# Kernel tuning notes

Measured on AMD Instinct MI355X. Metric: run time of the kernel, lower is better.

The kernel has to match this reference:

```python
import jax, jax.numpy as jnp
import numpy as np

N_NODES = 100000
N_EDGES = 1600000
IN_FEATS = 64
HIDDEN = 64
TOPO_DIM = 16
NUM_CLASSES = 4
NUM_GRAPHS = 64


def setup_inputs() -> dict:
    key = jax.random.key(0)
    ks = jax.random.split(key, 10)
    x = jax.random.normal(ks[0], (N_NODES, IN_FEATS), dtype=jnp.float32)
    edge_index = jax.random.randint(ks[1], (2, N_EDGES), 0, N_NODES, dtype=jnp.int64)
    batch = jnp.sort(jax.random.randint(ks[2], (N_NODES,), 0, NUM_GRAPHS, dtype=jnp.int64))
    topo = jax.random.normal(ks[3], (NUM_GRAPHS, TOPO_DIM), dtype=jnp.float32)
    # GCNConv weights (glorot-ish scale) and biases
    W1 = jax.random.normal(ks[4], (IN_FEATS, HIDDEN), dtype=jnp.float32) / np.sqrt(IN_FEATS)
    b1 = jnp.zeros((HIDDEN,), dtype=jnp.float32)
    W2 = jax.random.normal(ks[5], (HIDDEN, HIDDEN), dtype=jnp.float32) / np.sqrt(HIDDEN)
    b2 = jnp.zeros((HIDDEN,), dtype=jnp.float32)
    Wlin = jax.random.normal(ks[6], (HIDDEN + TOPO_DIM, NUM_CLASSES), dtype=jnp.float32) / np.sqrt(HIDDEN + TOPO_DIM)
    blin = jnp.zeros((NUM_CLASSES,), dtype=jnp.float32)
    return {"x": x, "edge_index": edge_index, "batch": batch, "topo": topo,
            "W1": W1, "b1": b1, "W2": W2, "b2": b2, "Wlin": Wlin, "blin": blin}


def _gcn_conv(x, W, b, src, dst, deg_inv_sqrt):
    # PyG GCNConv: add self-loops, symmetric normalization D^-1/2 (A+I) D^-1/2, then linear.
    xw = x @ W                                   # [N, H]
    norm = deg_inv_sqrt[src] * deg_inv_sqrt[dst]  # [E]
    msgs = xw[src] * norm[:, None]               # gather + scale, [E, H]
    agg = jax.ops.segment_sum(msgs, dst, num_segments=x.shape[0])
    # self-loop contribution: norm_ii = deg_inv_sqrt[i]^2
    agg = agg + xw * (deg_inv_sqrt * deg_inv_sqrt)[:, None]
    return agg + b


def reference(x, edge_index, batch, topo, W1, b1, W2, b2, Wlin, blin):
    src, dst = edge_index[0], edge_index[1]
    n = x.shape[0]
    # degree including self-loop
    deg = jax.ops.segment_sum(jnp.ones_like(dst, dtype=x.dtype), dst, num_segments=n) + 1.0
    deg_inv_sqrt = jax.lax.rsqrt(deg)
    h = jax.nn.relu(_gcn_conv(x, W1, b1, src, dst, deg_inv_sqrt))
    # F.dropout(p=0.5, training=False) -> identity at inference
    h = jax.nn.relu(_gcn_conv(h, W2, b2, src, dst, deg_inv_sqrt))
    # global mean pool over graphs
    sums = jax.ops.segment_sum(h, batch, num_segments=NUM_GRAPHS)
    counts = jax.ops.segment_sum(jnp.ones((n,), dtype=h.dtype), batch, num_segments=NUM_GRAPHS)
    g = sums / jnp.maximum(counts, 1.0)[:, None]  # [G, H]
    gtopo = jnp.concatenate([g, topo], axis=1)    # [G, H + topo_dim]
    return gtopo @ Wlin + blin
```

## Files before the change

### kernel.cpp

```cpp
#include <hip/hip_runtime.h>
#include <hip/hip_bf16.h>

#define NGRAPH  64
#define TOPO_D  16
#define NBLK    512
#define MAXB    512
#define GROWS   8
#define PCH     16

typedef float v2f __attribute__((ext_vector_type(2)));

static __device__ __forceinline__ unsigned f2bf(float f) {
    unsigned u = __float_as_uint(f);
    return (u + 0x7FFFu + ((u >> 16) & 1u)) >> 16;
}
static __device__ __forceinline__ float bf_lo(unsigned u) { return __uint_as_float(u << 16); }
static __device__ __forceinline__ float bf_hi(unsigned u) { return __uint_as_float(u & 0xFFFF0000u); }

static __device__ __forceinline__ void gemm_rows_bf(
        const float* __restrict__ X, const float* Wreg,
        unsigned short* __restrict__ Abf, int row0, int N, int lane) {
    #pragma unroll
    for (int j = 0; j < GROWS; ++j) {
        int row = row0 + j;
        if (row >= N) return;
        const float* xr = X + (size_t)row * 64;
        float acc = 0.0f;
        #pragma unroll
        for (int k = 0; k < 64; ++k) acc = fmaf(xr[k], Wreg[k], acc);
        Abf[(size_t)row * 64 + lane] = (unsigned short)f2bf(acc);
    }
}

static __device__ __forceinline__ void gemm_rows_fp8(
        const unsigned* __restrict__ X32, const float* Wreg,
        unsigned* __restrict__ A8, const float* __restrict__ dis,
        int row0, int N, int lane) {
    #pragma unroll
    for (int j = 0; j < GROWS; ++j) {
        int row = row0 + j;
        if (row >= N) return;
        const unsigned* xr = X32 + (size_t)row * 32;
        float acc = 0.0f;
        #pragma unroll
        for (int k = 0; k < 32; ++k) {
            unsigned u = xr[k];
            acc = fmaf(bf_lo(u), Wreg[2 * k], acc);
            acc = fmaf(bf_hi(u), Wreg[2 * k + 1], acc);
        }
        acc *= dis[row];
        float nb1 = __shfl_xor(acc, 1, 64);
        float lo = (lane & 1) ? nb1 : acc;
        float hi = (lane & 1) ? acc : nb1;
        int pk = __builtin_amdgcn_cvt_pk_fp8_f32(lo, hi, 0, false);
        int pk2 = __shfl_xor(pk, 2, 64);
        unsigned dw = (lane & 2) ? (((unsigned)pk2 & 0xFFFFu) | ((unsigned)pk << 16))
                                 : (((unsigned)pk & 0xFFFFu) | ((unsigned)pk2 << 16));
        if ((lane & 3) == 0) A8[(size_t)row * 16 + (lane >> 2)] = dw;
    }
}

__global__ __launch_bounds__(256) void hybrid_gemm_hist_kernel(
        const float* __restrict__ X, const float* __restrict__ W,
        unsigned short* __restrict__ Abf,
        const int* __restrict__ dst, int* __restrict__ bhist,
        int N, int E, int Gg, int nb2, int CE) {
    __shared__ int hist[MAXB];
    int t = threadIdx.x;
    if ((int)blockIdx.x < Gg) {
        int lane = t & 63;
        float Wreg[64];
        #pragma unroll
        for (int k = 0; k < 64; ++k) Wreg[k] = W[k * 64 + lane];
        int wave = __builtin_amdgcn_readfirstlane(blockIdx.x * 4 + (t >> 6));
        gemm_rows_bf(X, Wreg, Abf, wave * GROWS, N, lane);
    } else {
        int blk = blockIdx.x - Gg;
        for (int i = t; i < nb2; i += 256) hist[i] = 0;
        __syncthreads();
        int e0 = blk * CE, e1 = min(e0 + CE, E);
        for (int e = e0 + t; e < e1; e += 256) atomicAdd(&hist[dst[e] >> 8], 1);
        __syncthreads();
        for (int i = t; i < nb2; i += 256) bhist[blk * nb2 + i] = hist[i];
    }
}

__global__ __launch_bounds__(256) void scan_cols_kernel(
        int* __restrict__ bhist, int* __restrict__ ctot, int nb2) {
    __shared__ int sd[256];
    int c = blockIdx.x;
    int t = threadIdx.x;
    int v0 = bhist[t * nb2 + c];
    int v1 = bhist[(t + 256) * nb2 + c];
    int tsum = v0 + v1;
    sd[t] = tsum; __syncthreads();
    for (int off = 1; off < 256; off <<= 1) {
        int u = (t >= off) ? sd[t - off] : 0;
        __syncthreads();
        sd[t] += u;
        __syncthreads();
    }
    int excl = sd[t] - tsum;
    bhist[t * nb2 + c] = excl;
    bhist[(t + 256) * nb2 + c] = excl + v0;
    if (t == 255) ctot[c] = sd[255];
}

__global__ void scan_gstart_kernel(const int* __restrict__ ctot, int* __restrict__ cbase,
                                   const int* __restrict__ batch, int* __restrict__ gstart,
                                   int nb2, int N) {
    if (blockIdx.x == 0) {
        int lane = threadIdx.x;
        if (lane >= 64) return;
        int base = lane * 8;
        int vals[8];
        int s = 0;
        #pragma unroll
        for (int k = 0; k < 8; ++k) {
            int i = base + k;
            int v = (i < nb2) ? ctot[i] : 0;
            vals[k] = s; s += v;
        }
        int inc = s;
        for (int off = 1; off < 64; off <<= 1) {
            int u = __shfl_up(inc, off, 64);
            if (lane >= off) inc += u;
        }
        int lexcl = inc - s;
        #pragma unroll
        for (int k = 0; k < 8; ++k) {
            int i = base + k;
            if (i <= nb2) cbase[i] = lexcl + vals[k];
        }
    } else {
        int g = threadIdx.x;
        if (g > NGRAPH) return;
        int lo = 0, hi = N;
        while (lo < hi) {
            int mid = (lo + hi) >> 1;
            if (batch[mid] < g) lo = mid + 1; else hi = mid;
        }
        gstart[g] = lo;
    }
}

__global__ __launch_bounds__(256) void scatter_sorted_kernel(
        const int* __restrict__ src, const int* __restrict__ dst,
        const int* __restrict__ bhist, const int* __restrict__ cbase,
        unsigned* __restrict__ ebuf, int E, int nb2, int CE) {
    __shared__ int cur[MAXB];
    int blk = blockIdx.x, t = threadIdx.x;
    for (int i = t; i < nb2; i += 256) cur[i] = bhist[blk * nb2 + i] + cbase[i];
    __syncthreads();
    int e0 = blk * CE, e1 = min(e0 + CE, E);
    for (int e = e0 + t; e < e1; e += 256) {
        int d = dst[e];
        int pos = atomicAdd(&cur[d >> 8], 1);
        ebuf[pos] = ((unsigned)src[e] << 8) | (unsigned)(d & 255);
    }
}

__global__ __launch_bounds__(256) void build_csr_kernel(
        const unsigned* __restrict__ ebuf, const int* __restrict__ cbase,
        int* __restrict__ col, int* __restrict__ rowptr,
        int* __restrict__ degi, float* __restrict__ dis,
        const unsigned* __restrict__ Abf32, unsigned* __restrict__ A8, int N) {
    __shared__ int cnt[256];
    __shared__ int loff[256];
    __shared__ float disS[256];
    int b = blockIdx.x, t = threadIdx.x;
    int e0 = cbase[b], e1 = cbase[b + 1];
    cnt[t] = 0; __syncthreads();
    for (int i = e0 + t; i < e1; i += 256) atomicAdd(&cnt[ebuf[i] & 255u], 1);
    __syncthreads();
    int v = cnt[t];
    loff[t] = v; __syncthreads();
    for (int off = 1; off < 256; off <<= 1) {
        int u = (t >= off) ? loff[t - off] : 0;
        __syncthreads();
        loff[t] += u;
        __syncthreads();
    }
    int excl = loff[t] - v;
    int node = b * 256 + t;
    float ds = rsqrtf((float)v + 1.0f);
    disS[t] = ds;
    if (node < N) {
        degi[node]   = v;
        dis[node]    = ds;
        rowptr[node] = e0 + excl;
    }
    __syncthreads();
    cnt[t] = excl;
    __syncthreads();
    for (int i = e0 + t; i < e1; i += 256) {
        unsigned p = ebuf[i];
        int pos = atomicAdd(&cnt[p & 255u], 1);
        col[e0 + pos] = (int)(p >> 8);
    }
    int base8 = b * 256 * 16;
    for (int i = t; i < 256 * 16; i += 256) {
        int r = i >> 4;
        int dwo = i & 15;
        int nd = b * 256 + r;
        if (nd < N) {
            float d2 = disS[r];
            unsigned u0 = Abf32[(size_t)nd * 32 + dwo * 2];
            unsigned u1 = Abf32[(size_t)nd * 32 + dwo * 2 + 1];
            int dw = __builtin_amdgcn_cvt_pk_fp8_f32(bf_lo(u0) * d2, bf_hi(u0) * d2, 0, false);
            dw = __builtin_amdgcn_cvt_pk_fp8_f32(bf_lo(u1) * d2, bf_hi(u1) * d2, dw, true);
            A8[base8 + i] = (unsigned)dw;
        }
    }
}

static __device__ __forceinline__ void gather_node(
        const unsigned* __restrict__ A8, const int* __restrict__ col,
        int beg, int deg, int node, int f8, float acc[8]) {
    const char* Abase = (const char*)A8 + f8 * 8;
    uint2 an = *(const uint2*)(Abase + ((size_t)node << 6));
    v2f a0 = __builtin_amdgcn_cvt_pk_f32_fp8(an.x, false);
    v2f a1 = __builtin_amdgcn_cvt_pk_f32_fp8(an.x, true);
    v2f a2 = __builtin_amdgcn_cvt_pk_f32_fp8(an.y, false);
    v2f a3 = __builtin_amdgcn_cvt_pk_f32_fp8(an.y, true);
    acc[0] = a0.x; acc[1] = a0.y; acc[2] = a1.x; acc[3] = a1.y;
    acc[4] = a2.x; acc[5] = a2.y; acc[6] = a3.x; acc[7] = a3.y;
    int j = 0;
    for (; j + 4 <= deg; j += 4) {
        int s0 = col[beg + j]     << 6;
        int s1 = col[beg + j + 1] << 6;
        int s2 = col[beg + j + 2] << 6;
        int s3 = col[beg + j + 3] << 6;
        uint2 v0 = *(const uint2*)(Abase + s0);
        uint2 v1 = *(const uint2*)(Abase + s1);
        uint2 v2 = *(const uint2*)(Abase + s2);
        uint2 v3 = *(const uint2*)(Abase + s3);
        v2f f0, f1, f2, f3;
        f0 = __builtin_amdgcn_cvt_pk_f32_fp8(v0.x, false); acc[0] += f0.x; acc[1] += f0.y;
        f1 = __builtin_amdgcn_cvt_pk_f32_fp8(v0.x, true);  acc[2] += f1.x; acc[3] += f1.y;
        f2 = __builtin_amdgcn_cvt_pk_f32_fp8(v0.y, false); acc[4] += f2.x; acc[5] += f2.y;
        f3 = __builtin_amdgcn_cvt_pk_f32_fp8(v0.y, true);  acc[6] += f3.x; acc[7] += f3.y;
        f0 = __builtin_amdgcn_cvt_pk_f32_fp8(v1.x, false); acc[0] += f0.x; acc[1] += f0.y;
        f1 = __builtin_amdgcn_cvt_pk_f32_fp8(v1.x, true);  acc[2] += f1.x; acc[3] += f1.y;
        f2 = __builtin_amdgcn_cvt_pk_f32_fp8(v1.y, false); acc[4] += f2.x; acc[5] += f2.y;
        f3 = __builtin_amdgcn_cvt_pk_f32_fp8(v1.y, true);  acc[6] += f3.x; acc[7] += f3.y;
        f0 = __builtin_amdgcn_cvt_pk_f32_fp8(v2.x, false); acc[0] += f0.x; acc[1] += f0.y;
        f1 = __builtin_amdgcn_cvt_pk_f32_fp8(v2.x, true);  acc[2] += f1.x; acc[3] += f1.y;
        f2 = __builtin_amdgcn_cvt_pk_f32_fp8(v2.y, false); acc[4] += f2.x; acc[5] += f2.y;
        f3 = __builtin_amdgcn_cvt_pk_f32_fp8(v2.y, true);  acc[6] += f3.x; acc[7] += f3.y;
        f0 = __builtin_amdgcn_cvt_pk_f32_fp8(v3.x, false); acc[0] += f0.x; acc[1] += f0.y;
        f1 = __builtin_amdgcn_cvt_pk_f32_fp8(v3.x, true);  acc[2] += f1.x; acc[3] += f1.y;
        f2 = __builtin_amdgcn_cvt_pk_f32_fp8(v3.y, false); acc[4] += f2.x; acc[5] += f2.y;
        f3 = __builtin_amdgcn_cvt_pk_f32_fp8(v3.y, true);  acc[6] += f3.x; acc[7] += f3.y;
    }
    for (; j < deg; ++j) {
        int s = col[beg + j] << 6;
        uint2 v = *(const uint2*)(Abase + s);
        v2f f0 = __builtin_amdgcn_cvt_pk_f32_fp8(v.x, false);
        v2f f1 = __builtin_amdgcn_cvt_pk_f32_fp8(v.x, true);
        v2f f2 = __builtin_amdgcn_cvt_pk_f32_fp8(v.y, false);
        v2f f3 = __builtin_amdgcn_cvt_pk_f32_fp8(v.y, true);
        acc[0] += f0.x; acc[1] += f0.y; acc[2] += f1.x; acc[3] += f1.y;
        acc[4] += f2.x; acc[5] += f2.y; acc[6] += f3.x; acc[7] += f3.y;
    }
}

__global__ __launch_bounds__(256) void pull_csr_kernel(
        const unsigned* __restrict__ A8, unsigned* __restrict__ Bbf,
        const int* __restrict__ rowptr, const int* __restrict__ degi,
        const float* __restrict__ dis, const float* __restrict__ bias,
        const int* __restrict__ col, int N) {
    int wave = (blockIdx.x * blockDim.x + threadIdx.x) >> 6;
    int lane = threadIdx.x & 63;
    int i = lane >> 3;
    int f8 = lane & 7;
    int node = wave * 8 + i;
    bool valid = node < N;
    if (!valid) node = N - 1;
    int deg = degi[node];
    int beg = rowptr[node];
    float acc[8];
    gather_node(A8, col, beg, deg, node, f8, acc);
    float d = dis[node];
    float4 b0 = ((const float4*)bias)[f8 * 2];
    float4 b1 = ((const float4*)bias)[f8 * 2 + 1];
    float r[8];
    r[0] = fmaxf(d * acc[0] + b0.x, 0.f);
    r[1] = fmaxf(d * acc[1] + b0.y, 0.f);
    r[2] = fmaxf(d * acc[2] + b0.z, 0.f);
    r[3] = fmaxf(d * acc[3] + b0.w, 0.f);
    r[4] = fmaxf(d * acc[4] + b1.x, 0.f);
    r[5] = fmaxf(d * acc[5] + b1.y, 0.f);
    r[6] = fmaxf(d * acc[6] + b1.z, 0.f);
    r[7] = fmaxf(d * acc[7] + b1.w, 0.f);
    if (valid) {
        uint4 o;
        o.x = f2bf(r[0]) | (f2bf(r[1]) << 16);
        o.y = f2bf(r[2]) | (f2bf(r[3]) << 16);
        o.z = f2bf(r[4]) | (f2bf(r[5]) << 16);
        o.w = f2bf(r[6]) | (f2bf(r[7]) << 16);
        *(uint4*)(Bbf + (size_t)node * 32 + f8 * 4) = o;
    }
}

__global__ __launch_bounds__(256) void pull2_csr_kernel(
        const unsigned* __restrict__ A8, float* __restrict__ B,
        const int* __restrict__ rowptr, const int* __restrict__ degi,
        const float* __restrict__ dis, const float* __restrict__ bias,
        const int* __restrict__ col, int N) {
    int wave = (blockIdx.x * blockDim.x + threadIdx.x) >> 6;
    int lane = threadIdx.x & 63;
    int i = lane >> 3;
    int f8 = lane & 7;
    int node = wave * 8 + i;
    bool valid = node < N;
    if (!valid) node = N - 1;
    int deg = degi[node];
    int beg = rowptr[node];
    float acc[8];
    gather_node(A8, col, beg, deg, node, f8, acc);
    float d = dis[node];
    float4 b0 = ((const float4*)bias)[f8 * 2];
    float4 b1 = ((const float4*)bias)[f8 * 2 + 1];
    float4 r0, r1;
    r0.x = fmaxf(d * acc[0] + b0.x, 0.f);
    r0.y = fmaxf(d * acc[1] + b0.y, 0.f);
    r0.z = fmaxf(d * acc[2] + b0.z, 0.f);
    r0.w = fmaxf(d * acc[3] + b0.w, 0.f);
    r1.x = fmaxf(d * acc[4] + b1.x, 0.f);
    r1.y = fmaxf(d * acc[5] + b1.y, 0.f);
    r1.z = fmaxf(d * acc[6] + b1.z, 0.f);
    r1.w = fmaxf(d * acc[7] + b1.w, 0.f);
    if (valid) {
        *(float4*)(B + (size_t)node * 64 + f8 * 8)     = r0;
        *(float4*)(B + (size_t)node * 64 + f8 * 8 + 4) = r1;
    }
}

__global__ __launch_bounds__(256) void gemm_scale_kernel(
        const unsigned* __restrict__ X32, const float* __restrict__ W,
        const float* __restrict__ dis, unsigned* __restrict__ A8, int N) {
    int lane = threadIdx.x & 63;
    float Wreg[64];
    #pragma unroll
    for (int k = 0; k < 64; ++k) Wreg[k] = W[k * 64 + lane];
    int wave = __builtin_amdgcn_readfirstlane(blockIdx.x * 4 + (threadIdx.x >> 6));
    gemm_rows_fp8(X32, Wreg, A8, dis, wave * GROWS, N, lane);
}

__global__ __launch_bounds__(256) void pool2_kernel(
        const float* __restrict__ H, const int* __restrict__ gstart,
        float* __restrict__ gsum) {
    __shared__ float red[4][64];
    int b = blockIdx.x;
    int g = b >> 4;
    int c = b & 15;
    int s = gstart[g], e = gstart[g + 1];
    int len = e - s;
    int chunk = (len + PCH - 1) / PCH;
    int lo = s + c * chunk;
    int hi = min(lo + chunk, e);
    int w = threadIdx.x >> 6;
    int lane = threadIdx.x & 63;
    float acc0 = 0.f, acc1 = 0.f;
    int n = lo + w;
    for (; n + 4 < hi; n += 8) {
        acc0 += H[(size_t)n * 64 + lane];
        acc1 += H[(size_t)(n + 4) * 64 + lane];
    }
    if (n < hi) acc0 += H[(size_t)n * 64 + lane];
    red[w][lane] = acc0 + acc1;
    __syncthreads();
    if (threadIdx.x < 64) {
        float v = red[0][threadIdx.x] + red[1][threadIdx.x]
                + red[2][threadIdx.x] + red[3][threadIdx.x];
        unsafeAtomicAdd(&gsum[g * 64 + threadIdx.x], v);
    }
}

__global__ __launch_bounds__(256) void head_kernel(
        const float* __restrict__ gsum, const int* __restrict__ gstart,
        const float* __restrict__ topo, const float* __restrict__ Wlin,
        const float* __restrict__ blin, float* __restrict__ out) {
    int t = threadIdx.x;
    int g = t >> 2;
    int c = t & 3;
    float cntf = (float)(gstart[g + 1] - gstart[g]);
    float inv = 1.0f / fmaxf(cntf, 1.0f);
    float v = blin[c];
    #pragma unroll
    for (int f = 0; f < 64; ++f) v += gsum[g * 64 + f] * inv * Wlin[f * 4 + c];
    #pragma unroll
    for (int t2 = 0; t2 < TOPO_D; ++t2) v += topo[g * TOPO_D + t2] * Wlin[(64 + t2) * 4 + c];
    out[g * 4 + c] = v;
}

extern "C" void kernel_launch(void* const* d_in, const int* in_sizes, int n_in,
                              void* d_out, int out_size, void* d_ws, size_t ws_size,
                              hipStream_t stream) {
    const float* x     = (const float*)d_in[0];
    const int*   ei    = (const int*)d_in[1];
    const int*   batch = (const int*)d_in[2];
    const float* topo  = (const float*)d_in[3];
    const float* W1    = (const float*)d_in[4];
    const float* b1    = (const float*)d_in[5];
    const float* W2    = (const float*)d_in[6];
    const float* b2    = (const float*)d_in[7];
    const float* Wlin  = (const float*)d_in[8];
    const float* blin  = (const float*)d_in[9];
    float* out = (float*)d_out;

    const int N = in_sizes[0] / 64;
    const int E = in_sizes[1] / 2;
    const int* src = ei;
    const int* dst = ei + E;
    const int nb2 = (N + 255) / 256;
    const int CE  = (E + NBLK - 1) / NBLK;

    char* ws = (char*)d_ws;
    size_t off = 0;
    unsigned short* Abf = (unsigned short*)(ws + off); off += (size_t)N * 64 * 2;
    unsigned* Bbf    = (unsigned*)(ws + off); off += (size_t)N * 32 * 4;
    unsigned* A8     = (unsigned*)(ws + off); off += (size_t)N * 64;
    float*    B2     = (float*)   (ws + off); off += (size_t)N * 64 * 4;
    int*      col    = (int*)     (ws + off); off += (size_t)E * 4;
    unsigned* ebuf   = (unsigned*)(ws + off); off += (size_t)E * 4;
    int*      bhist  = (int*)     (ws + off); off += (size_t)NBLK * nb2 * 4;
    int*      ctot   = (int*)     (ws + off); off += (size_t)(nb2 + 8) * 4;
    int*      cbase  = (int*)     (ws + off); off += (size_t)(nb2 + 8) * 4;
    int*      rowptr = (int*)     (ws + off); off += (size_t)(N + 1) * 4;
    int*      degi   = (int*)     (ws + off); off += (size_t)N * 4;
    float*    dis    = (float*)   (ws + off); off += (size_t)N * 4;
    int*      gstart = (int*)     (ws + off); off += (size_t)(NGRAPH + 8) * 4;
    float*    gsum   = (float*)   (ws + off); off += (size_t)NGRAPH * 64 * 4;

    hipMemsetAsync(gsum, 0, (size_t)NGRAPH * 64 * 4, stream);

    const int nWaves = (N + GROWS - 1) / GROWS;
    const int Gg = (nWaves + 3) / 4;
    hybrid_gemm_hist_kernel<<<Gg + NBLK, 256, 0, stream>>>(x, W1, Abf, dst, bhist, N, E, Gg, nb2, CE);
    scan_cols_kernel<<<nb2, 256, 0, stream>>>(bhist, ctot, nb2);
    scan_gstart_kernel<<<2, 256, 0, stream>>>(ctot, cbase, batch, gstart, nb2, N);
    scatter_sorted_kernel<<<NBLK, 256, 0, stream>>>(src, dst, bhist, cbase, ebuf, E, nb2, CE);
    build_csr_kernel<<<nb2, 256, 0, stream>>>(ebuf, cbase, col, rowptr, degi, dis,
                                              (const unsigned*)Abf, A8, N);

    int pullBlocks = ((N + 7) / 8 + 3) / 4;
    pull_csr_kernel<<<pullBlocks, 256, 0, stream>>>(A8, Bbf, rowptr, degi, dis, b1, col, N);

    gemm_scale_kernel<<<Gg, 256, 0, stream>>>(Bbf, W2, dis, A8, N);
    pull2_csr_kernel<<<pullBlocks, 256, 0, stream>>>(A8, B2, rowptr, degi, dis, b2, col, N);

    pool2_kernel<<<NGRAPH * PCH, 256, 0, stream>>>(B2, gstart, gsum);
    head_kernel<<<1, 256, 0, stream>>>(gsum, gstart, topo, Wlin, blin, out);
}
```

Baseline: 241.0 us.

## Fuse layer-1 aggregation with W2 GEMM and layer-2 aggregation with mean pooling

The layer-1 pull kernel now stages each wave's 8 bf16 output rows in shared memory and immediately multiplies them by W2, writing the fp8 scaled features directly. This removes the Bbf round trip and the separate GEMM launch. The layer-2 pull kernel now reduces node outputs into per-graph sums with wave shuffles and atomics, which removes the fp32 B2 buffer write/read and the pool kernel. In exchange, the fused kernels hold more registers (W2 in registers) and issue more atomics where a wave's nodes span a graph boundary.

```diff
diff --git a/kernel.cpp b/kernel.cpp
--- a/kernel.cpp
+++ b/kernel.cpp
@@ -6,7 +6,6 @@
 #define NBLK    512
 #define MAXB    512
 #define GROWS   8
-#define PCH     16
 
 typedef float v2f __attribute__((ext_vector_type(2)));
 
@@ -29,34 +28,6 @@
         #pragma unroll
         for (int k = 0; k < 64; ++k) acc = fmaf(xr[k], Wreg[k], acc);
         Abf[(size_t)row * 64 + lane] = (unsigned short)f2bf(acc);
-    }
-}
-
-static __device__ __forceinline__ void gemm_rows_fp8(
-        const unsigned* __restrict__ X32, const float* Wreg,
-        unsigned* __restrict__ A8, const float* __restrict__ dis,
-        int row0, int N, int lane) {
-    #pragma unroll
-    for (int j = 0; j < GROWS; ++j) {
-        int row = row0 + j;
-        if (row >= N) return;
-        const unsigned* xr = X32 + (size_t)row * 32;
-        float acc = 0.0f;
-        #pragma unroll
-        for (int k = 0; k < 32; ++k) {
-            unsigned u = xr[k];
-            acc = fmaf(bf_lo(u), Wreg[2 * k], acc);
-            acc = fmaf(bf_hi(u), Wreg[2 * k + 1], acc);
-        }
-        acc *= dis[row];
-        float nb1 = __shfl_xor(acc, 1, 64);
-        float lo = (lane & 1) ? nb1 : acc;
-        float hi = (lane & 1) ? acc : nb1;
-        int pk = __builtin_amdgcn_cvt_pk_fp8_f32(lo, hi, 0, false);
-        int pk2 = __shfl_xor(pk, 2, 64);
-        unsigned dw = (lane & 2) ? (((unsigned)pk2 & 0xFFFFu) | ((unsigned)pk << 16))
-                                 : (((unsigned)pk & 0xFFFFu) | ((unsigned)pk2 << 16));
-        if ((lane & 3) == 0) A8[(size_t)row * 16 + (lane >> 2)] = dw;
     }
 }
 
@@ -265,22 +236,92 @@
     }
 }
 
-__global__ __launch_bounds__(256) void pull_csr_kernel(
-        const unsigned* __restrict__ A8, unsigned* __restrict__ Bbf,
-        const int* __restrict__ rowptr, const int* __restrict__ degi,
-        const float* __restrict__ dis, const float* __restrict__ bias,
-        const int* __restrict__ col, int N) {
-    int wave = (blockIdx.x * blockDim.x + threadIdx.x) >> 6;
+__global__ __launch_bounds__(256) void pull1_gemm_kernel(
+        const unsigned* __restrict__ A8a, const int* __restrict__ rowptr,
+        const int* __restrict__ degi, const float* __restrict__ dis,
+        const float* __restrict__ bias, const int* __restrict__ col,
+        const float* __restrict__ W2, unsigned* __restrict__ A8b, int N) {
+    __shared__ __align__(16) unsigned hl[4][8][32];
+    int w = threadIdx.x >> 6;
+    int waveg = (blockIdx.x * blockDim.x + threadIdx.x) >> 6;
     int lane = threadIdx.x & 63;
     int i = lane >> 3;
     int f8 = lane & 7;
-    int node = wave * 8 + i;
+    int node = waveg * 8 + i;
     bool valid = node < N;
     if (!valid) node = N - 1;
     int deg = degi[node];
     int beg = rowptr[node];
     float acc[8];
-    gather_node(A8, col, beg, deg, node, f8, acc);
+    gather_node(A8a, col, beg, deg, node, f8, acc);
+    float d = dis[node];
+    float4 b0 = ((const float4*)bias)[f8 * 2];
+    float4 b1 = ((const float4*)bias)[f8 * 2 + 1];
+    float r0 = fmaxf(d * acc[0] + b0.x, 0.f);
+    float r1 = fmaxf(d * acc[1] + b0.y, 0.f);
+    float r2 = fmaxf(d * acc[2] + b0.z, 0.f);
+    float r3 = fmaxf(d * acc[3] + b0.w, 0.f);
+    float r4 = fmaxf(d * acc[4] + b1.x, 0.f);
+    float r5 = fmaxf(d * acc[5] + b1.y, 0.f);
+    float r6 = fmaxf(d * acc[6] + b1.z, 0.f);
+    float r7 = fmaxf(d * acc[7] + b1.w, 0.f);
+    uint4 o;
+    o.x = f2bf(r0) | (f2bf(r1) << 16);
+    o.y = f2bf(r2) | (f2bf(r3) << 16);
+    o.z = f2bf(r4) | (f2bf(r5) << 16);
+    o.w = f2bf(r6) | (f2bf(r7) << 16);
+    *(uint4*)&hl[w][i][f8 * 4] = o;
+    __syncthreads();
+    float Wreg[64];
+    #pragma unroll
+    for (int k = 0; k < 64; ++k) Wreg[k] = W2[k * 64 + lane];
+    int row0 = __builtin_amdgcn_readfirstlane(waveg) * 8;
+    #pragma unroll
+    for (int j = 0; j < 8; ++j) {
+        int row = row0 + j;
+        if (row >= N) break;
+        const uint4* xr4 = (const uint4*)&hl[w][j][0];
+        float a2 = 0.0f;
+        #pragma unroll
+        for (int k4 = 0; k4 < 8; ++k4) {
+            uint4 u4 = xr4[k4];
+            a2 = fmaf(bf_lo(u4.x), Wreg[8 * k4 + 0], a2);
+            a2 = fmaf(bf_hi(u4.x), Wreg[8 * k4 + 1], a2);
+            a2 = fmaf(bf_lo(u4.y), Wreg[8 * k4 + 2], a2);
+            a2 = fmaf(bf_hi(u4.y), Wreg[8 * k4 + 3], a2);
+            a2 = fmaf(bf_lo(u4.z), Wreg[8 * k4 + 4], a2);
+            a2 = fmaf(bf_hi(u4.z), Wreg[8 * k4 + 5], a2);
+            a2 = fmaf(bf_lo(u4.w), Wreg[8 * k4 + 6], a2);
+            a2 = fmaf(bf_hi(u4.w), Wreg[8 * k4 + 7], a2);
+        }
+        a2 *= dis[row];
+        float nb1 = __shfl_xor(a2, 1, 64);
+        float lo = (lane & 1) ? nb1 : a2;
+        float hi = (lane & 1) ? a2 : nb1;
+        int pk = __builtin_amdgcn_cvt_pk_fp8_f32(lo, hi, 0, false);
+        int pk2 = __shfl_xor(pk, 2, 64);
+        unsigned dw = (lane & 2) ? (((unsigned)pk2 & 0xFFFFu) | ((unsigned)pk << 16))
+                                 : (((unsigned)pk & 0xFFFFu) | ((unsigned)pk2 << 16));
+        if ((lane & 3) == 0) A8b[(size_t)row * 16 + (lane >> 2)] = dw;
+    }
+}
+
+__global__ __launch_bounds__(256) void pull2_pool_kernel(
+        const unsigned* __restrict__ A8b, const int* __restrict__ rowptr,
+        const int* __restrict__ degi, const float* __restrict__ dis,
+        const float* __restrict__ bias, const int* __restrict__ col,
+        const int* __restrict__ batch, float* __restrict__ gsum, int N) {
+    int waveg = (blockIdx.x * blockDim.x + threadIdx.x) >> 6;
+    int lane = threadIdx.x & 63;
+    int i = lane >> 3;
+    int f8 = lane & 7;
+    int node = waveg * 8 + i;
+    bool valid = node < N;
+    if (!valid) node = N - 1;
+    int deg = degi[node];
+    int beg = rowptr[node];
+    float acc[8];
+    gather_node(A8b, col, beg, deg, node, f8, acc);
     float d = dis[node];
     float4 b0 = ((const float4*)bias)[f8 * 2];
     float4 b1 = ((const float4*)bias)[f8 * 2 + 1];
@@ -293,88 +334,29 @@
     r[5] = fmaxf(d * acc[5] + b1.y, 0.f);
     r[6] = fmaxf(d * acc[6] + b1.z, 0.f);
     r[7] = fmaxf(d * acc[7] + b1.w, 0.f);
-    if (valid) {
-        uint4 o;
-        o.x = f2bf(r[0]) | (f2bf(r[1]) << 16);
-        o.y = f2bf(r[2]) | (f2bf(r[3]) << 16);
-        o.z = f2bf(r[4]) | (f2bf(r[5]) << 16);
-        o.w = f2bf(r[6]) | (f2bf(r[7]) << 16);
-        *(uint4*)(Bbf + (size_t)node * 32 + f8 * 4) = o;
-    }
-}
-
-__global__ __launch_bounds__(256) void pull2_csr_kernel(
-        const unsigned* __restrict__ A8, float* __restrict__ B,
-        const int* __restrict__ rowptr, const int* __restrict__ degi,
-        const float* __restrict__ dis, const float* __restrict__ bias,
-        const int* __restrict__ col, int N) {
-    int wave = (blockIdx.x * blockDim.x + threadIdx.x) >> 6;
-    int lane = threadIdx.x & 63;
-    int i = lane >> 3;
-    int f8 = lane & 7;
-    int node = wave * 8 + i;
-    bool valid = node < N;
-    if (!valid) node = N - 1;
-    int deg = degi[node];
-    int beg = rowptr[node];
-    float acc[8];
-    gather_node(A8, col, beg, deg, node, f8, acc);
-    float d = dis[node];
-    float4 b0 = ((const float4*)bias)[f8 * 2];
-    float4 b1 = ((const float4*)bias)[f8 * 2 + 1];
-    float4 r0, r1;
-    r0.x = fmaxf(d * acc[0] + b0.x, 0.f);
-    r0.y = fmaxf(d * acc[1] + b0.y, 0.f);
-    r0.z = fmaxf(d * acc[2] + b0.z, 0.f);
-    r0.w = fmaxf(d * acc[3] + b0.w, 0.f);
-    r1.x = fmaxf(d * acc[4] + b1.x, 0.f);
-    r1.y = fmaxf(d * acc[5] + b1.y, 0.f);
-    r1.z = fmaxf(d * acc[6] + b1.z, 0.f);
-    r1.w = fmaxf(d * acc[7] + b1.w, 0.f);
-    if (valid) {
-        *(float4*)(B + (size_t)node * 64 + f8 * 8)     = r0;
-        *(float4*)(B + (size_t)node * 64 + f8 * 8 + 4) = r1;
-    }
-}
-
-__global__ __launch_bounds__(256) void gemm_scale_kernel(
-        const unsigned* __restrict__ X32, const float* __restrict__ W,
-        const float* __restrict__ dis, unsigned* __restrict__ A8, int N) {
-    int lane = threadIdx.x & 63;
-    float Wreg[64];
-    #pragma unroll
-    for (int k = 0; k < 64; ++k) Wreg[k] = W[k * 64 + lane];
-    int wave = __builtin_amdgcn_readfirstlane(blockIdx.x * 4 + (threadIdx.x >> 6));
-    gemm_rows_fp8(X32, Wreg, A8, dis, wave * GROWS, N, lane);
-}
-
-__global__ __launch_bounds__(256) void pool2_kernel(
-        const float* __restrict__ H, const int* __restrict__ gstart,
-        float* __restrict__ gsum) {
-    __shared__ float red[4][64];
-    int b = blockIdx.x;
-    int g = b >> 4;
-    int c = b & 15;
-    int s = gstart[g], e = gstart[g + 1];
-    int len = e - s;
-    int chunk = (len + PCH - 1) / PCH;
-    int lo = s + c * chunk;
-    int hi = min(lo + chunk, e);
-    int w = threadIdx.x >> 6;
-    int lane = threadIdx.x & 63;
-    float acc0 = 0.f, acc1 = 0.f;
-    int n = lo + w;
-    for (; n + 4 < hi; n += 8) {
-        acc0 += H[(size_t)n * 64 + lane];
-        acc1 += H[(size_t)(n + 4) * 64 + lane];
-    }
-    if (n < hi) acc0 += H[(size_t)n * 64 + lane];
-    red[w][lane] = acc0 + acc1;
-    __syncthreads();
-    if (threadIdx.x < 64) {
-        float v = red[0][threadIdx.x] + red[1][threadIdx.x]
-                + red[2][threadIdx.x] + red[3][threadIdx.x];
-        unsafeAtomicAdd(&gsum[g * 64 + threadIdx.x], v);
+    if (!valid) {
+        #pragma unroll
+        for (int j = 0; j < 8; ++j) r[j] = 0.f;
+    }
+    int g = batch[node];
+    int gFirst = __shfl(g, 0, 64);
+    int gLast  = __shfl(g, 63, 64);
+    if (gFirst == gLast) {
+        #pragma unroll
+        for (int j = 0; j < 8; ++j) {
+            r[j] += __shfl_xor(r[j], 8, 64);
+            r[j] += __shfl_xor(r[j], 16, 64);
+            r[j] += __shfl_xor(r[j], 32, 64);
+        }
+        if (i == 0) {
+            #pragma unroll
+            for (int j = 0; j < 8; ++j)
+                unsafeAtomicAdd(&gsum[gFirst * 64 + f8 * 8 + j], r[j]);
+        }
+    } else {
+        #pragma unroll
+        for (int j = 0; j < 8; ++j)
+            unsafeAtomicAdd(&gsum[g * 64 + f8 * 8 + j], r[j]);
     }
 }
 
@@ -420,9 +402,8 @@
     char* ws = (char*)d_ws;
     size_t off = 0;
     unsigned short* Abf = (unsigned short*)(ws + off); off += (size_t)N * 64 * 2;
-    unsigned* Bbf    = (unsigned*)(ws + off); off += (size_t)N * 32 * 4;
-    unsigned* A8     = (unsigned*)(ws + off); off += (size_t)N * 64;
-    float*    B2     = (float*)   (ws + off); off += (size_t)N * 64 * 4;
+    unsigned* A8a    = (unsigned*)(ws + off); off += (size_t)N * 64;
+    unsigned* A8b    = (unsigned*)(ws + off); off += (size_t)N * 64;
     int*      col    = (int*)     (ws + off); off += (size_t)E * 4;
     unsigned* ebuf   = (unsigned*)(ws + off); off += (size_t)E * 4;
     int*      bhist  = (int*)     (ws + off); off += (size_t)NBLK * nb2 * 4;
@@ -443,14 +424,13 @@
     scan_gstart_kernel<<<2, 256, 0, stream>>>(ctot, cbase, batch, gstart, nb2, N);
     scatter_sorted_kernel<<<NBLK, 256, 0, stream>>>(src, dst, bhist, cbase, ebuf, E, nb2, CE);
     build_csr_kernel<<<nb2, 256, 0, stream>>>(ebuf, cbase, col, rowptr, degi, dis,
-                                              (const unsigned*)Abf, A8, N);
+                                              (const unsigned*)Abf, A8a, N);
 
     int pullBlocks = ((N + 7) / 8 + 3) / 4;
-    pull_csr_kernel<<<pullBlocks, 256, 0, stream>>>(A8, Bbf, rowptr, degi, dis, b1, col, N);
-
-    gemm_scale_kernel<<<Gg, 256, 0, stream>>>(Bbf, W2, dis, A8, N);
-    pull2_csr_kernel<<<pullBlocks, 256, 0, stream>>>(A8, B2, rowptr, degi, dis, b2, col, N);
-
-    pool2_kernel<<<NGRAPH * PCH, 256, 0, stream>>>(B2, gstart, gsum);
+    pull1_gemm_kernel<<<pullBlocks, 256, 0, stream>>>(A8a, rowptr, degi, dis, b1, col, W2, A8b, N);
+
+    pull2_pool_kernel<<<pullBlocks, 256, 0, stream>>>(A8b, rowptr, degi, dis, b2, col,
+                                                      batch, gsum, N);
+
     head_kernel<<<1, 256, 0, stream>>>(gsum, gstart, topo, Wlin, blin, out);
 }
```

Result: slower. 346.4 us (+43.7%).

## Fuse second-layer pull with global mean pooling via wave-reduced atomics

Applied to the files above, without the earlier changes.

The second GCN aggregation kernel now accumulates its ReLU output directly into the per-graph sums instead of writing a full N×64 fp32 buffer that a separate pool kernel then re-reads. When all 8 nodes of a wave share a graph id, the values are reduced across lanes with shuffles and one lane group issues atomics; otherwise each lane issues its own atomics. This removes a large intermediate write and read and one kernel launch, but adds atomic traffic onto a small 64×64 sum array, which could contend heavily.

```diff
diff --git a/kernel.cpp b/kernel.cpp
--- a/kernel.cpp
+++ b/kernel.cpp
@@ -6,7 +6,6 @@
 #define NBLK    512
 #define MAXB    512
 #define GROWS   8
-#define PCH     16
 
 typedef float v2f __attribute__((ext_vector_type(2)));
 
@@ -284,30 +283,40 @@
     float d = dis[node];
     float4 b0 = ((const float4*)bias)[f8 * 2];
     float4 b1 = ((const float4*)bias)[f8 * 2 + 1];
-    float r[8];
-    r[0] = fmaxf(d * acc[0] + b0.x, 0.f);
-    r[1] = fmaxf(d * acc[1] + b0.y, 0.f);
-    r[2] = fmaxf(d * acc[2] + b0.z, 0.f);
-    r[3] = fmaxf(d * acc[3] + b0.w, 0.f);
-    r[4] = fmaxf(d * acc[4] + b1.x, 0.f);
-    r[5] = fmaxf(d * acc[5] + b1.y, 0.f);
-    r[6] = fmaxf(d * acc[6] + b1.z, 0.f);
-    r[7] = fmaxf(d * acc[7] + b1.w, 0.f);
+    float r0 = fmaxf(d * acc[0] + b0.x, 0.f);
+    float r1 = fmaxf(d * acc[1] + b0.y, 0.f);
+    float r2 = fmaxf(d * acc[2] + b0.z, 0.f);
+    float r3 = fmaxf(d * acc[3] + b0.w, 0.f);
+    float r4 = fmaxf(d * acc[4] + b1.x, 0.f);
+    float r5 = fmaxf(d * acc[5] + b1.y, 0.f);
+    float r6 = fmaxf(d * acc[6] + b1.z, 0.f);
+    float r7 = fmaxf(d * acc[7] + b1.w, 0.f);
     if (valid) {
         uint4 o;
-        o.x = f2bf(r[0]) | (f2bf(r[1]) << 16);
-        o.y = f2bf(r[2]) | (f2bf(r[3]) << 16);
-        o.z = f2bf(r[4]) | (f2bf(r[5]) << 16);
-        o.w = f2bf(r[6]) | (f2bf(r[7]) << 16);
+        o.x = f2bf(r0) | (f2bf(r1) << 16);
+        o.y = f2bf(r2) | (f2bf(r3) << 16);
+        o.z = f2bf(r4) | (f2bf(r5) << 16);
+        o.w = f2bf(r6) | (f2bf(r7) << 16);
         *(uint4*)(Bbf + (size_t)node * 32 + f8 * 4) = o;
     }
 }
 
-__global__ __launch_bounds__(256) void pull2_csr_kernel(
-        const unsigned* __restrict__ A8, float* __restrict__ B,
-        const int* __restrict__ rowptr, const int* __restrict__ degi,
-        const float* __restrict__ dis, const float* __restrict__ bias,
-        const int* __restrict__ col, int N) {
+__global__ __launch_bounds__(256) void gemm_scale_kernel(
+        const unsigned* __restrict__ X32, const float* __restrict__ W,
+        const float* __restrict__ dis, unsigned* __restrict__ A8, int N) {
+    int lane = threadIdx.x & 63;
+    float Wreg[64];
+    #pragma unroll
+    for (int k = 0; k < 64; ++k) Wreg[k] = W[k * 64 + lane];
+    int wave = __builtin_amdgcn_readfirstlane(blockIdx.x * 4 + (threadIdx.x >> 6));
+    gemm_rows_fp8(X32, Wreg, A8, dis, wave * GROWS, N, lane);
+}
+
+__global__ __launch_bounds__(256) void pull2_pool_kernel(
+        const unsigned* __restrict__ A8, const int* __restrict__ rowptr,
+        const int* __restrict__ degi, const float* __restrict__ dis,
+        const float* __restrict__ bias, const int* __restrict__ col,
+        const int* __restrict__ batch, float* __restrict__ gsum, int N) {
     int wave = (blockIdx.x * blockDim.x + threadIdx.x) >> 6;
     int lane = threadIdx.x & 63;
     int i = lane >> 3;
@@ -322,59 +331,48 @@
     float d = dis[node];
     float4 b0 = ((const float4*)bias)[f8 * 2];
     float4 b1 = ((const float4*)bias)[f8 * 2 + 1];
-    float4 r0, r1;
-    r0.x = fmaxf(d * acc[0] + b0.x, 0.f);
-    r0.y = fmaxf(d * acc[1] + b0.y, 0.f);
-    r0.z = fmaxf(d * acc[2] + b0.z, 0.f);
-    r0.w = fmaxf(d * acc[3] + b0.w, 0.f);
-    r1.x = fmaxf(d * acc[4] + b1.x, 0.f);
-    r1.y = fmaxf(d * acc[5] + b1.y, 0.f);
-    r1.z = fmaxf(d * acc[6] + b1.z, 0.f);
-    r1.w = fmaxf(d * acc[7] + b1.w, 0.f);
-    if (valid) {
-        *(float4*)(B + (size_t)node * 64 + f8 * 8)     = r0;
-        *(float4*)(B + (size_t)node * 64 + f8 * 8 + 4) = r1;
-    }
-}
-
-__global__ __launch_bounds__(256) void gemm_scale_kernel(
-        const unsigned* __restrict__ X32, const float* __restrict__ W,
-        const float* __restrict__ dis, unsigned* __restrict__ A8, int N) {
-    int lane = threadIdx.x & 63;
-    float Wreg[64];
-    #pragma unroll
-    for (int k = 0; k < 64; ++k) Wreg[k] = W[k * 64 + lane];
-    int wave = __builtin_amdgcn_readfirstlane(blockIdx.x * 4 + (threadIdx.x >> 6));
-    gemm_rows_fp8(X32, Wreg, A8, dis, wave * GROWS, N, lane);
-}
-
-__global__ __launch_bounds__(256) void pool2_kernel(
-        const float* __restrict__ H, const int* __restrict__ gstart,
-        float* __restrict__ gsum) {
-    __shared__ float red[4][64];
-    int b = blockIdx.x;
-    int g = b >> 4;
-    int c = b & 15;
-    int s = gstart[g], e = gstart[g + 1];
-    int len = e - s;
-    int chunk = (len + PCH - 1) / PCH;
-    int lo = s + c * chunk;
-    int hi = min(lo + chunk, e);
-    int w = threadIdx.x >> 6;
-    int lane = threadIdx.x & 63;
-    float acc0 = 0.f, acc1 = 0.f;
-    int n = lo + w;
-    for (; n + 4 < hi; n += 8) {
-        acc0 += H[(size_t)n * 64 + lane];
-        acc1 += H[(size_t)(n + 4) * 64 + lane];
-    }
-    if (n < hi) acc0 += H[(size_t)n * 64 + lane];
-    red[w][lane] = acc0 + acc1;
-    __syncthreads();
-    if (threadIdx.x < 64) {
-        float v = red[0][threadIdx.x] + red[1][threadIdx.x]
-                + red[2][threadIdx.x] + red[3][threadIdx.x];
-        unsafeAtomicAdd(&gsum[g * 64 + threadIdx.x], v);
+    float h0 = fmaxf(d * acc[0] + b0.x, 0.f);
+    float h1 = fmaxf(d * acc[1] + b0.y, 0.f);
+    float h2 = fmaxf(d * acc[2] + b0.z, 0.f);
+    float h3 = fmaxf(d * acc[3] + b0.w, 0.f);
+    float h4 = fmaxf(d * acc[4] + b1.x, 0.f);
+    float h5 = fmaxf(d * acc[5] + b1.y, 0.f);
+    float h6 = fmaxf(d * acc[6] + b1.z, 0.f);
+    float h7 = fmaxf(d * acc[7] + b1.w, 0.f);
+    if (!valid) { h0 = 0.f; h1 = 0.f; h2 = 0.f; h3 = 0.f; h4 = 0.f; h5 = 0.f; h6 = 0.f; h7 = 0.f; }
+    int g = batch[node];
+    int gF = __shfl(g, 0, 64);
+    int gL = __shfl(g, 63, 64);
+    if (gF == gL) {
+        h0 += __shfl_xor(h0, 8, 64); h0 += __shfl_xor(h0, 16, 64); h0 += __shfl_xor(h0, 32, 64);
+        h1 += __shfl_xor(h1, 8, 64); h1 += __shfl_xor(h1, 16, 64); h1 += __shfl_xor(h1, 32, 64);
+        h2 += __shfl_xor(h2, 8, 64); h2 += __shfl_xor(h2, 16, 64); h2 += __shfl_xor(h2, 32, 64);
+        h3 += __shfl_xor(h3, 8, 64); h3 += __shfl_xor(h3, 16, 64); h3 += __shfl_xor(h3, 32, 64);
+        h4 += __shfl_xor(h4, 8, 64); h4 += __shfl_xor(h4, 16, 64); h4 += __shfl_xor(h4, 32, 64);
+        h5 += __shfl_xor(h5, 8, 64); h5 += __shfl_xor(h5, 16, 64); h5 += __shfl_xor(h5, 32, 64);
+        h6 += __shfl_xor(h6, 8, 64); h6 += __shfl_xor(h6, 16, 64); h6 += __shfl_xor(h6, 32, 64);
+        h7 += __shfl_xor(h7, 8, 64); h7 += __shfl_xor(h7, 16, 64); h7 += __shfl_xor(h7, 32, 64);
+        if (i == 0) {
+            float* gp = gsum + gF * 64 + f8 * 8;
+            unsafeAtomicAdd(gp + 0, h0);
+            unsafeAtomicAdd(gp + 1, h1);
+            unsafeAtomicAdd(gp + 2, h2);
+            unsafeAtomicAdd(gp + 3, h3);
+            unsafeAtomicAdd(gp + 4, h4);
+            unsafeAtomicAdd(gp + 5, h5);
+            unsafeAtomicAdd(gp + 6, h6);
+            unsafeAtomicAdd(gp + 7, h7);
+        }
+    } else {
+        float* gp = gsum + g * 64 + f8 * 8;
+        unsafeAtomicAdd(gp + 0, h0);
+        unsafeAtomicAdd(gp + 1, h1);
+        unsafeAtomicAdd(gp + 2, h2);
+        unsafeAtomicAdd(gp + 3, h3);
+        unsafeAtomicAdd(gp + 4, h4);
+        unsafeAtomicAdd(gp + 5, h5);
+        unsafeAtomicAdd(gp + 6, h6);
+        unsafeAtomicAdd(gp + 7, h7);
     }
 }
 
@@ -422,7 +420,6 @@
     unsigned short* Abf = (unsigned short*)(ws + off); off += (size_t)N * 64 * 2;
     unsigned* Bbf    = (unsigned*)(ws + off); off += (size_t)N * 32 * 4;
     unsigned* A8     = (unsigned*)(ws + off); off += (size_t)N * 64;
-    float*    B2     = (float*)   (ws + off); off += (size_t)N * 64 * 4;
     int*      col    = (int*)     (ws + off); off += (size_t)E * 4;
     unsigned* ebuf   = (unsigned*)(ws + off); off += (size_t)E * 4;
     int*      bhist  = (int*)     (ws + off); off += (size_t)NBLK * nb2 * 4;
@@ -449,8 +446,8 @@
     pull_csr_kernel<<<pullBlocks, 256, 0, stream>>>(A8, Bbf, rowptr, degi, dis, b1, col, N);
 
     gemm_scale_kernel<<<Gg, 256, 0, stream>>>(Bbf, W2, dis, A8, N);
-    pull2_csr_kernel<<<pullBlocks, 256, 0, stream>>>(A8, B2, rowptr, degi, dis, b2, col, N);
-
-    pool2_kernel<<<NGRAPH * PCH, 256, 0, stream>>>(B2, gstart, gsum);
+    pull2_pool_kernel<<<pullBlocks, 256, 0, stream>>>(A8, rowptr, degi, dis, b2, col,
+                                                      batch, gsum, N);
+
     head_kernel<<<1, 256, 0, stream>>>(gsum, gstart, topo, Wlin, blin, out);
 }
```

Result: slower. 364.6 us (+51.3%).
